# Kernel optimization log

Measured on AMD Instinct MI355X. Metric: run time of the kernel, lower is better.

The kernel has to match this reference:

```python
import jax, jax.numpy as jnp
import numpy as np

IN_C = 512
OUT_C = 1024
N = 8192


def _xavier(key, shape):
    fan_in, fan_out = shape[1], shape[0]
    limit = float(np.sqrt(6.0 / (fan_in + fan_out)))
    return jax.random.uniform(key, shape, jnp.float32, -limit, limit)


def setup_inputs() -> dict:
    key = jax.random.key(0)
    ks = jax.random.split(key, 20)
    inp = {
        'x': jax.random.normal(ks[0], (IN_C, N), jnp.float32),
        'c_prev_dim0': jax.random.normal(ks[1], (OUT_C, N), jnp.float32),
        'h_prev_dim0': jax.random.normal(ks[2], (OUT_C, N), jnp.float32),
        'c_prev_dim1': jax.random.normal(ks[3], (OUT_C, N), jnp.float32),
        'h_prev_dim1': jax.random.normal(ks[4], (OUT_C, N), jnp.float32),
    }
    names_x = ['w_ii', 'w_if', 'w_ig', 'w_io']
    names_h = ['w_hi', 'w_hf', 'w_hg', 'w_ho']
    names_b = ['b_i', 'b_f', 'b_g', 'b_o']
    k = 5
    for n in names_x:
        inp[n] = _xavier(ks[k], (OUT_C, IN_C)); k += 1
    for n in names_h:
        inp[n] = _xavier(ks[k], (OUT_C, OUT_C)); k += 1
    for n in names_b:
        inp[n] = _xavier(ks[k], (OUT_C, 1)); k += 1
    inp['weighted_sum'] = jax.random.uniform(ks[k], (2,), jnp.float32)
    return inp


def reference(x, c_prev_dim0, h_prev_dim0, c_prev_dim1, h_prev_dim1,
              w_ii, w_if, w_ig, w_io,
              w_hi, w_hf, w_hg, w_ho,
              b_i, b_f, b_g, b_o,
              weighted_sum):
    # Input projections shared by both spatial directions: (out, N)
    xi = w_ii @ x
    xf = w_if @ x
    xg = w_ig @ x
    xo = w_io @ x

    def gates(h_prev, c_prev):
        i = jax.nn.sigmoid(xi + w_hi @ h_prev + b_i)
        f = jax.nn.sigmoid(xf + w_hf @ h_prev + b_f)
        g = jnp.tanh(xg + w_hg @ h_prev + b_g)
        o = jax.nn.sigmoid(xo + w_ho @ h_prev + b_o)
        c = f * c_prev + i * g
        h = o * jnp.tanh(c)
        return c, h

    ct0, ht0 = gates(h_prev_dim0, c_prev_dim0)
    ct1, ht1 = gates(h_prev_dim1, c_prev_dim1)
    ct = ct0 * weighted_sum[0] + ct1 * weighted_sum[1]
    ht = ht0 * weighted_sum[0] + ht1 * weighted_sum[1]
    return ct, ht
```

## Files before the change

### kernel.cpp

```cpp
#include <hip/hip_runtime.h>
#include <cstdint>
#include <cstddef>

#define IN_C  512
#define OUT_C 1024
#define NSAMP 8192

#define BM 64
#define BN 64
#define BK 64

typedef __bf16 bf16x8 __attribute__((ext_vector_type(8)));
typedef float  f32x4  __attribute__((ext_vector_type(4)));

__device__ __forceinline__ unsigned short f2bf(float f) {
    unsigned int u = __float_as_uint(f);
    u += 0x7FFFu + ((u >> 16) & 1u);
    return (unsigned short)(u >> 16);
}

__device__ __forceinline__ float sigmoid_f(float x) {
    return 1.0f / (1.0f + __expf(-x));
}
__device__ __forceinline__ float tanh_f(float x) {
    float e = __expf(2.0f * x);
    return 1.0f - 2.0f / (e + 1.0f);
}

__global__ void tcvt_kernel(const float* __restrict__ in, unsigned short* __restrict__ out,
                            int R, int C) {
    __shared__ float t[32][33];
    const int tx = threadIdx.x;
    const int ty = threadIdx.y;
    const int c0 = blockIdx.x * 32;
    const int r0 = blockIdx.y * 32;
#pragma unroll
    for (int i = 0; i < 4; ++i)
        t[ty + i * 8][tx] = in[(size_t)(r0 + ty + i * 8) * C + (c0 + tx)];
    __syncthreads();
#pragma unroll
    for (int i = 0; i < 4; ++i)
        out[(size_t)(c0 + ty + i * 8) * R + (r0 + tx)] = f2bf(t[tx][ty + i * 8]);
}

__global__ void cvt_kernel(const float* __restrict__ in, unsigned short* __restrict__ out, int n4) {
    int idx = blockIdx.x * blockDim.x + threadIdx.x;
    if (idx < n4) {
        float4 v = reinterpret_cast<const float4*>(in)[idx];
        ushort4 o;
        o.x = f2bf(v.x); o.y = f2bf(v.y); o.z = f2bf(v.z); o.w = f2bf(v.w);
        reinterpret_cast<ushort4*>(out)[idx] = o;
    }
}

__global__ __launch_bounds__(256, 2) void mdlstm_main(
    const unsigned short* __restrict__ xT,
    const unsigned short* __restrict__ h0T,
    const unsigned short* __restrict__ h1T,
    const unsigned short* __restrict__ wx,
    const unsigned short* __restrict__ wh,
    const float* __restrict__ b_i, const float* __restrict__ b_f,
    const float* __restrict__ b_g, const float* __restrict__ b_o,
    const float* __restrict__ cp0, const float* __restrict__ cp1,
    const float* __restrict__ wsum,
    float* __restrict__ out)
{
    __shared__ __align__(16) unsigned char smem[6 * 8192];

    const int tid  = threadIdx.x;
    const int lane = tid & 63;
    const int wid  = tid >> 6;
    const int wm   = wid >> 1;
    const int wn   = wid & 1;
    const int g4   = lane >> 4;
    const int l16  = lane & 15;

    const int brow = blockIdx.y * BM;
    const int bcol = blockIdx.x * BN;

    f32x4 acc[2][4][2][2];
#pragma unroll
    for (int d = 0; d < 2; ++d)
#pragma unroll
        for (int q = 0; q < 4; ++q)
#pragma unroll
            for (int a = 0; a < 2; ++a)
#pragma unroll
                for (int b = 0; b < 2; ++b)
                    acc[d][q][a][b] = (f32x4){0.f, 0.f, 0.f, 0.f};

    auto stage_tile = [&](const unsigned short* gbase, int pitch_bytes, int k0bytes, int lds_base) {
#pragma unroll
        for (int j = 0; j < 2; ++j) {
            const int slot = wid * 2 + j;
            const int u    = slot * 1024 + lane * 16;
            const int row  = u >> 7;
            const int kb   = u & 127;
            const char* src = (const char*)gbase + (size_t)row * pitch_bytes + k0bytes
                              + (kb ^ ((row & 7) << 4));
            __builtin_amdgcn_global_load_lds((const unsigned int*)src,
                                             (unsigned int*)(smem + lds_base + slot * 1024),
                                             16, 0, 0);
        }
    };

    auto frag_at = [&](int lds_base, int row, int kbyte) -> bf16x8 {
        const int off = lds_base + row * 128 + (kbyte ^ ((row & 7) << 4));
        return *reinterpret_cast<const bf16x8*>(smem + off);
    };

    for (int st = 0; st < IN_C / BK; ++st) {
        const int k0b = st * BK * 2;
#pragma unroll
        for (int q = 0; q < 4; ++q)
            stage_tile(wx + (size_t)q * OUT_C * IN_C + (size_t)brow * IN_C, IN_C * 2, k0b, q * 8192);
        stage_tile(xT + (size_t)bcol * IN_C, IN_C * 2, k0b, 4 * 8192);
        __syncthreads();
#pragma unroll
        for (int kk = 0; kk < 2; ++kk) {
            const int kbyte = kk * 64 + g4 * 16;
            bf16x8 afr[4][2], bfr[2];
#pragma unroll
            for (int q = 0; q < 4; ++q)
#pragma unroll
                for (int fm = 0; fm < 2; ++fm)
                    afr[q][fm] = frag_at(q * 8192, wm * 32 + fm * 16 + l16, kbyte);
#pragma unroll
            for (int fn = 0; fn < 2; ++fn)
                bfr[fn] = frag_at(4 * 8192, wn * 32 + fn * 16 + l16, kbyte);
#pragma unroll
            for (int q = 0; q < 4; ++q)
#pragma unroll
                for (int fm = 0; fm < 2; ++fm)
#pragma unroll
                    for (int fn = 0; fn < 2; ++fn)
                        acc[0][q][fm][fn] = __builtin_amdgcn_mfma_f32_16x16x32_bf16(
                            afr[q][fm], bfr[fn], acc[0][q][fm][fn], 0, 0, 0);
        }
        __syncthreads();
    }

#pragma unroll
    for (int q = 0; q < 4; ++q)
#pragma unroll
        for (int a = 0; a < 2; ++a)
#pragma unroll
            for (int b = 0; b < 2; ++b)
                acc[1][q][a][b] = acc[0][q][a][b];

    for (int st = 0; st < OUT_C / BK; ++st) {
        const int k0b = st * BK * 2;
#pragma unroll
        for (int q = 0; q < 4; ++q)
            stage_tile(wh + (size_t)q * OUT_C * OUT_C + (size_t)brow * OUT_C, OUT_C * 2, k0b, q * 8192);
        stage_tile(h0T + (size_t)bcol * OUT_C, OUT_C * 2, k0b, 4 * 8192);
        stage_tile(h1T + (size_t)bcol * OUT_C, OUT_C * 2, k0b, 5 * 8192);
        __syncthreads();
#pragma unroll
        for (int kk = 0; kk < 2; ++kk) {
            const int kbyte = kk * 64 + g4 * 16;
            bf16x8 afr[4][2], b0f[2], b1f[2];
#pragma unroll
            for (int q = 0; q < 4; ++q)
#pragma unroll
                for (int fm = 0; fm < 2; ++fm)
                    afr[q][fm] = frag_at(q * 8192, wm * 32 + fm * 16 + l16, kbyte);
#pragma unroll
            for (int fn = 0; fn < 2; ++fn) {
                b0f[fn] = frag_at(4 * 8192, wn * 32 + fn * 16 + l16, kbyte);
                b1f[fn] = frag_at(5 * 8192, wn * 32 + fn * 16 + l16, kbyte);
            }
#pragma unroll
            for (int q = 0; q < 4; ++q)
#pragma unroll
                for (int fm = 0; fm < 2; ++fm)
#pragma unroll
                    for (int fn = 0; fn < 2; ++fn) {
                        acc[0][q][fm][fn] = __builtin_amdgcn_mfma_f32_16x16x32_bf16(
                            afr[q][fm], b0f[fn], acc[0][q][fm][fn], 0, 0, 0);
                        acc[1][q][fm][fn] = __builtin_amdgcn_mfma_f32_16x16x32_bf16(
                            afr[q][fm], b1f[fn], acc[1][q][fm][fn], 0, 0, 0);
                    }
        }
        __syncthreads();
    }

    const float w0 = wsum[0], w1 = wsum[1];
#pragma unroll
    for (int fm = 0; fm < 2; ++fm)
#pragma unroll
        for (int fn = 0; fn < 2; ++fn)
#pragma unroll
            for (int r = 0; r < 4; ++r) {
                const int m = brow + wm * 32 + fm * 16 + g4 * 4 + r;
                const int n = bcol + wn * 32 + fn * 16 + l16;
                const size_t idx = (size_t)m * NSAMP + n;
                const float bi = b_i[m], bff = b_f[m], bg = b_g[m], bo = b_o[m];

                float c0v, h0v, c1v, h1v;
                {
                    float i_ = sigmoid_f(acc[0][0][fm][fn][r] + bi);
                    float f_ = sigmoid_f(acc[0][1][fm][fn][r] + bff);
                    float g_ = tanh_f   (acc[0][2][fm][fn][r] + bg);
                    float o_ = sigmoid_f(acc[0][3][fm][fn][r] + bo);
                    float c_ = f_ * cp0[idx] + i_ * g_;
                    c0v = c_;
                    h0v = o_ * tanh_f(c_);
                }
                {
                    float i_ = sigmoid_f(acc[1][0][fm][fn][r] + bi);
                    float f_ = sigmoid_f(acc[1][1][fm][fn][r] + bff);
                    float g_ = tanh_f   (acc[1][2][fm][fn][r] + bg);
                    float o_ = sigmoid_f(acc[1][3][fm][fn][r] + bo);
                    float c_ = f_ * cp1[idx] + i_ * g_;
                    c1v = c_;
                    h1v = o_ * tanh_f(c_);
                }
                out[idx] = w0 * c0v + w1 * c1v;
                out[(size_t)OUT_C * NSAMP + idx] = w0 * h0v + w1 * h1v;
            }
}

extern "C" void kernel_launch(void* const* d_in, const int* in_sizes, int n_in,
                              void* d_out, int out_size, void* d_ws, size_t ws_size,
                              hipStream_t stream) {
    (void)in_sizes; (void)n_in; (void)out_size; (void)ws_size;

    const float* x    = (const float*)d_in[0];
    const float* cp0  = (const float*)d_in[1];
    const float* hp0  = (const float*)d_in[2];
    const float* cp1  = (const float*)d_in[3];
    const float* hp1  = (const float*)d_in[4];
    const float* wxp[4] = {(const float*)d_in[5], (const float*)d_in[6],
                           (const float*)d_in[7], (const float*)d_in[8]};
    const float* whp[4] = {(const float*)d_in[9], (const float*)d_in[10],
                           (const float*)d_in[11], (const float*)d_in[12]};
    const float* b_i  = (const float*)d_in[13];
    const float* b_f  = (const float*)d_in[14];
    const float* b_g  = (const float*)d_in[15];
    const float* b_o  = (const float*)d_in[16];
    const float* wsum = (const float*)d_in[17];
    float* out = (float*)d_out;

    char* ws = (char*)d_ws;
    unsigned short* xT  = (unsigned short*)(ws);
    unsigned short* h0T = (unsigned short*)(ws + (size_t)8  * 1024 * 1024);
    unsigned short* h1T = (unsigned short*)(ws + (size_t)24 * 1024 * 1024);
    unsigned short* wxc = (unsigned short*)(ws + (size_t)40 * 1024 * 1024);
    unsigned short* whc = (unsigned short*)(ws + (size_t)44 * 1024 * 1024);

    dim3 tb(32, 8);
    tcvt_kernel<<<dim3(NSAMP / 32, IN_C  / 32), tb, 0, stream>>>(x,   xT,  IN_C,  NSAMP);
    tcvt_kernel<<<dim3(NSAMP / 32, OUT_C / 32), tb, 0, stream>>>(hp0, h0T, OUT_C, NSAMP);
    tcvt_kernel<<<dim3(NSAMP / 32, OUT_C / 32), tb, 0, stream>>>(hp1, h1T, OUT_C, NSAMP);

    for (int q = 0; q < 4; ++q)
        cvt_kernel<<<(OUT_C * IN_C / 4) / 256, 256, 0, stream>>>(
            wxp[q], wxc + (size_t)q * OUT_C * IN_C, OUT_C * IN_C / 4);
    for (int q = 0; q < 4; ++q)
        cvt_kernel<<<(OUT_C * OUT_C / 4) / 256, 256, 0, stream>>>(
            whp[q], whc + (size_t)q * OUT_C * OUT_C, OUT_C * OUT_C / 4);

    mdlstm_main<<<dim3(NSAMP / BN, OUT_C / BM), 256, 0, stream>>>(
        xT, h0T, h1T, wxc, whc, b_i, b_f, b_g, b_o, cp0, cp1, wsum, out);
}
```

Baseline: 250.2 us.

## Pack gate weights into unified K=1536 matrix and pipeline 256x128 tile GEMM

Concatenates the x and h weights of all four gates into one row-interleaved bf16 matrix with K=1536, packed by a single kernel. The main kernel becomes one larger-tile GEMM (256 gate rows by 128 samples for both directions) running 512 threads, with double-buffered LDS staging via global_load_lds, explicit vmcnt waits, barriers and setprio around the MFMAs. The two directions are reduced through LDS in the epilogue. The aim is more data reuse per tile, fewer launches, and overlap of memory with compute. The cost is 128KB of LDS per block, which limits occupancy, and hand-tuned synchronization that is fragile.

```diff
diff --git a/kernel.cpp b/kernel.cpp
--- a/kernel.cpp
+++ b/kernel.cpp
@@ -5,23 +5,19 @@
 #define IN_C  512
 #define OUT_C 1024
 #define NSAMP 8192
-
-#define BM 64
-#define BN 64
-#define BK 64
+#define KTOT  1536
 
 typedef __bf16 bf16x8 __attribute__((ext_vector_type(8)));
 typedef float  f32x4  __attribute__((ext_vector_type(4)));
+
+#define SBAR() __builtin_amdgcn_s_barrier()
 
 __device__ __forceinline__ unsigned short f2bf(float f) {
     unsigned int u = __float_as_uint(f);
     u += 0x7FFFu + ((u >> 16) & 1u);
     return (unsigned short)(u >> 16);
 }
-
-__device__ __forceinline__ float sigmoid_f(float x) {
-    return 1.0f / (1.0f + __expf(-x));
-}
+__device__ __forceinline__ float sigmoid_f(float x) { return 1.0f / (1.0f + __expf(-x)); }
 __device__ __forceinline__ float tanh_f(float x) {
     float e = __expf(2.0f * x);
     return 1.0f - 2.0f / (e + 1.0f);
@@ -30,10 +26,8 @@
 __global__ void tcvt_kernel(const float* __restrict__ in, unsigned short* __restrict__ out,
                             int R, int C) {
     __shared__ float t[32][33];
-    const int tx = threadIdx.x;
-    const int ty = threadIdx.y;
-    const int c0 = blockIdx.x * 32;
-    const int r0 = blockIdx.y * 32;
+    const int tx = threadIdx.x, ty = threadIdx.y;
+    const int c0 = blockIdx.x * 32, r0 = blockIdx.y * 32;
 #pragma unroll
     for (int i = 0; i < 4; ++i)
         t[ty + i * 8][tx] = in[(size_t)(r0 + ty + i * 8) * C + (c0 + tx)];
@@ -43,182 +37,210 @@
         out[(size_t)(c0 + ty + i * 8) * R + (r0 + tx)] = f2bf(t[tx][ty + i * 8]);
 }
 
-__global__ void cvt_kernel(const float* __restrict__ in, unsigned short* __restrict__ out, int n4) {
-    int idx = blockIdx.x * blockDim.x + threadIdx.x;
-    if (idx < n4) {
-        float4 v = reinterpret_cast<const float4*>(in)[idx];
-        ushort4 o;
-        o.x = f2bf(v.x); o.y = f2bf(v.y); o.z = f2bf(v.z); o.w = f2bf(v.w);
-        reinterpret_cast<ushort4*>(out)[idx] = o;
-    }
-}
-
-__global__ __launch_bounds__(256, 2) void mdlstm_main(
+__global__ void packA_kernel(const float* __restrict__ x0, const float* __restrict__ x1,
+                             const float* __restrict__ x2, const float* __restrict__ x3,
+                             const float* __restrict__ h0, const float* __restrict__ h1,
+                             const float* __restrict__ h2, const float* __restrict__ h3,
+                             unsigned short* __restrict__ Ap) {
+    const int idx = blockIdx.x * 256 + threadIdx.x;
+    const int m = idx / 192, k8 = idx % 192;
+    const int g = m & 3, r = m >> 2;
+    const float* src;
+    if (k8 < 64) {
+        const float* a = (g & 2) ? ((g & 1) ? x3 : x2) : ((g & 1) ? x1 : x0);
+        src = a + (size_t)r * IN_C + k8 * 8;
+    } else {
+        const float* a = (g & 2) ? ((g & 1) ? h3 : h2) : ((g & 1) ? h1 : h0);
+        src = a + (size_t)r * OUT_C + (k8 - 64) * 8;
+    }
+    float4 v0 = reinterpret_cast<const float4*>(src)[0];
+    float4 v1 = reinterpret_cast<const float4*>(src)[1];
+    ushort4 o0, o1;
+    o0.x = f2bf(v0.x); o0.y = f2bf(v0.y); o0.z = f2bf(v0.z); o0.w = f2bf(v0.w);
+    o1.x = f2bf(v1.x); o1.y = f2bf(v1.y); o1.z = f2bf(v1.z); o1.w = f2bf(v1.w);
+    ushort4* dst = reinterpret_cast<ushort4*>(Ap + (size_t)m * KTOT + k8 * 8);
+    dst[0] = o0; dst[1] = o1;
+}
+
+__global__ __launch_bounds__(512, 2) void mdlstm_main(
+    const unsigned short* __restrict__ Ap,
     const unsigned short* __restrict__ xT,
     const unsigned short* __restrict__ h0T,
     const unsigned short* __restrict__ h1T,
-    const unsigned short* __restrict__ wx,
-    const unsigned short* __restrict__ wh,
     const float* __restrict__ b_i, const float* __restrict__ b_f,
     const float* __restrict__ b_g, const float* __restrict__ b_o,
     const float* __restrict__ cp0, const float* __restrict__ cp1,
     const float* __restrict__ wsum,
     float* __restrict__ out)
 {
-    __shared__ __align__(16) unsigned char smem[6 * 8192];
+    __shared__ __align__(16) unsigned char smem[131072];
 
     const int tid  = threadIdx.x;
     const int lane = tid & 63;
     const int wid  = tid >> 6;
-    const int wm   = wid >> 1;
-    const int wn   = wid & 1;
+    const int wm   = wid >> 2;
+    const int wn   = wid & 3;
     const int g4   = lane >> 4;
     const int l16  = lane & 15;
 
-    const int brow = blockIdx.y * BM;
-    const int bcol = blockIdx.x * BN;
-
-    f32x4 acc[2][4][2][2];
-#pragma unroll
-    for (int d = 0; d < 2; ++d)
-#pragma unroll
-        for (int q = 0; q < 4; ++q)
-#pragma unroll
-            for (int a = 0; a < 2; ++a)
-#pragma unroll
-                for (int b = 0; b < 2; ++b)
-                    acc[d][q][a][b] = (f32x4){0.f, 0.f, 0.f, 0.f};
-
-    auto stage_tile = [&](const unsigned short* gbase, int pitch_bytes, int k0bytes, int lds_base) {
-#pragma unroll
-        for (int j = 0; j < 2; ++j) {
-            const int slot = wid * 2 + j;
-            const int u    = slot * 1024 + lane * 16;
-            const int row  = u >> 7;
-            const int kb   = u & 127;
-            const char* src = (const char*)gbase + (size_t)row * pitch_bytes + k0bytes
-                              + (kb ^ ((row & 7) << 4));
+    const int by    = blockIdx.y;
+    const int bcol  = blockIdx.x * 128;
+    const int browM = by * 256;
+
+    f32x4 acc[8][4];
+#pragma unroll
+    for (int mf = 0; mf < 8; ++mf)
+#pragma unroll
+        for (int nf = 0; nf < 4; ++nf)
+            acc[mf][nf] = (f32x4){0.f, 0.f, 0.f, 0.f};
+
+    auto stage_A = [&](int P, int hA, int j1) {
+#pragma unroll
+        for (int c = 0; c < 2; ++c) {
+            const int u    = c * 8192 + tid * 16;
+            const int rloc = (u >> 6) & 127;
+            const int kb   = (u & 63) ^ (((u >> 7) & 3) << 4);
+            const char* src = (const char*)Ap
+                + ((size_t)(browM + hA * 128 + rloc) * KTOT + j1 * 64 + c * 32) * 2 + kb;
             __builtin_amdgcn_global_load_lds((const unsigned int*)src,
-                                             (unsigned int*)(smem + lds_base + slot * 1024),
-                                             16, 0, 0);
-        }
-    };
-
-    auto frag_at = [&](int lds_base, int row, int kbyte) -> bf16x8 {
-        const int off = lds_base + row * 128 + (kbyte ^ ((row & 7) << 4));
-        return *reinterpret_cast<const bf16x8*>(smem + off);
-    };
-
-    for (int st = 0; st < IN_C / BK; ++st) {
-        const int k0b = st * BK * 2;
-#pragma unroll
-        for (int q = 0; q < 4; ++q)
-            stage_tile(wx + (size_t)q * OUT_C * IN_C + (size_t)brow * IN_C, IN_C * 2, k0b, q * 8192);
-        stage_tile(xT + (size_t)bcol * IN_C, IN_C * 2, k0b, 4 * 8192);
-        __syncthreads();
-#pragma unroll
-        for (int kk = 0; kk < 2; ++kk) {
-            const int kbyte = kk * 64 + g4 * 16;
-            bf16x8 afr[4][2], bfr[2];
-#pragma unroll
-            for (int q = 0; q < 4; ++q)
-#pragma unroll
-                for (int fm = 0; fm < 2; ++fm)
-                    afr[q][fm] = frag_at(q * 8192, wm * 32 + fm * 16 + l16, kbyte);
-#pragma unroll
-            for (int fn = 0; fn < 2; ++fn)
-                bfr[fn] = frag_at(4 * 8192, wn * 32 + fn * 16 + l16, kbyte);
-#pragma unroll
-            for (int q = 0; q < 4; ++q)
-#pragma unroll
-                for (int fm = 0; fm < 2; ++fm)
-#pragma unroll
-                    for (int fn = 0; fn < 2; ++fn)
-                        acc[0][q][fm][fn] = __builtin_amdgcn_mfma_f32_16x16x32_bf16(
-                            afr[q][fm], bfr[fn], acc[0][q][fm][fn], 0, 0, 0);
-        }
-        __syncthreads();
-    }
-
-#pragma unroll
-    for (int q = 0; q < 4; ++q)
-#pragma unroll
-        for (int a = 0; a < 2; ++a)
-#pragma unroll
-            for (int b = 0; b < 2; ++b)
-                acc[1][q][a][b] = acc[0][q][a][b];
-
-    for (int st = 0; st < OUT_C / BK; ++st) {
-        const int k0b = st * BK * 2;
-#pragma unroll
-        for (int q = 0; q < 4; ++q)
-            stage_tile(wh + (size_t)q * OUT_C * OUT_C + (size_t)brow * OUT_C, OUT_C * 2, k0b, q * 8192);
-        stage_tile(h0T + (size_t)bcol * OUT_C, OUT_C * 2, k0b, 4 * 8192);
-        stage_tile(h1T + (size_t)bcol * OUT_C, OUT_C * 2, k0b, 5 * 8192);
-        __syncthreads();
-#pragma unroll
-        for (int kk = 0; kk < 2; ++kk) {
-            const int kbyte = kk * 64 + g4 * 16;
-            bf16x8 afr[4][2], b0f[2], b1f[2];
-#pragma unroll
-            for (int q = 0; q < 4; ++q)
-#pragma unroll
-                for (int fm = 0; fm < 2; ++fm)
-                    afr[q][fm] = frag_at(q * 8192, wm * 32 + fm * 16 + l16, kbyte);
-#pragma unroll
-            for (int fn = 0; fn < 2; ++fn) {
-                b0f[fn] = frag_at(4 * 8192, wn * 32 + fn * 16 + l16, kbyte);
-                b1f[fn] = frag_at(5 * 8192, wn * 32 + fn * 16 + l16, kbyte);
+                (unsigned int*)(smem + P * 65536 + hA * 16384 + u), 16, 0, 0);
+        }
+    };
+    auto stage_B = [&](int P, int d, int j2) {
+#pragma unroll
+        for (int c = 0; c < 2; ++c) {
+            const int u    = c * 8192 + tid * 16;
+            const int rloc = (u >> 6) & 127;
+            const int kb   = (u & 63) ^ (((u >> 7) & 3) << 4);
+            const char* src;
+            if (j2 < 8) {
+                src = (const char*)xT + ((size_t)(bcol + rloc) * IN_C + j2 * 64 + c * 32) * 2 + kb;
+            } else {
+                const unsigned short* hsrc = d ? h1T : h0T;
+                src = (const char*)hsrc + ((size_t)(bcol + rloc) * OUT_C + (j2 - 8) * 64 + c * 32) * 2 + kb;
             }
-#pragma unroll
-            for (int q = 0; q < 4; ++q)
-#pragma unroll
-                for (int fm = 0; fm < 2; ++fm)
-#pragma unroll
-                    for (int fn = 0; fn < 2; ++fn) {
-                        acc[0][q][fm][fn] = __builtin_amdgcn_mfma_f32_16x16x32_bf16(
-                            afr[q][fm], b0f[fn], acc[0][q][fm][fn], 0, 0, 0);
-                        acc[1][q][fm][fn] = __builtin_amdgcn_mfma_f32_16x16x32_bf16(
-                            afr[q][fm], b1f[fn], acc[1][q][fm][fn], 0, 0, 0);
-                    }
-        }
-        __syncthreads();
+            __builtin_amdgcn_global_load_lds((const unsigned int*)src,
+                (unsigned int*)(smem + P * 65536 + 32768 + d * 16384 + u), 16, 0, 0);
+        }
+    };
+
+    auto swzb = [](int u) { return u ^ (((u >> 7) & 3) << 4); };
+    auto fragA = [&](int P, int mf, int kk) -> bf16x8 {
+        const int u = kk * 8192 + (mf * 16 + l16) * 64 + g4 * 16;
+        return *reinterpret_cast<const bf16x8*>(smem + P * 65536 + wm * 16384 + swzb(u));
+    };
+    auto fragB = [&](int P, int nf, int kk) -> bf16x8 {
+        const int u = kk * 8192 + ((wn & 1) * 64 + nf * 16 + l16) * 64 + g4 * 16;
+        return *reinterpret_cast<const bf16x8*>(smem + P * 65536 + 32768 + (wn >> 1) * 16384 + swzb(u));
+    };
+
+    auto ktile = [&](int j, int P, int PN, bool stA, bool stB, bool tail) {
+        bf16x8 bF[4][2], aF[2][2];
+        auto mfma_pair = [&](int M) {
+            __builtin_amdgcn_s_setprio(1);
+#pragma unroll
+            for (int kk = 0; kk < 2; ++kk)
+#pragma unroll
+                for (int mi = 0; mi < 2; ++mi)
+#pragma unroll
+                    for (int nf = 0; nf < 4; ++nf)
+                        acc[M + mi][nf] = __builtin_amdgcn_mfma_f32_16x16x32_bf16(
+                            aF[mi][kk], bF[nf][kk], acc[M + mi][nf], 0, 0, 0);
+            __builtin_amdgcn_s_setprio(0);
+        };
+#pragma unroll
+        for (int nf = 0; nf < 4; ++nf) { bF[nf][0] = fragB(P, nf, 0); bF[nf][1] = fragB(P, nf, 1); }
+#pragma unroll
+        for (int kk = 0; kk < 2; ++kk) { aF[0][kk] = fragA(P, 0, kk); aF[1][kk] = fragA(P, 1, kk); }
+        if (stA) stage_A(PN, 0, j + 1);
+        SBAR();
+        mfma_pair(0);
+        SBAR();
+#pragma unroll
+        for (int kk = 0; kk < 2; ++kk) { aF[0][kk] = fragA(P, 2, kk); aF[1][kk] = fragA(P, 3, kk); }
+        if (stA) stage_A(PN, 1, j + 1);
+        SBAR();
+        mfma_pair(2);
+        SBAR();
+#pragma unroll
+        for (int kk = 0; kk < 2; ++kk) { aF[0][kk] = fragA(P, 4, kk); aF[1][kk] = fragA(P, 5, kk); }
+        if (stB) stage_B(P, 0, j + 2);
+        SBAR();
+        mfma_pair(4);
+        SBAR();
+#pragma unroll
+        for (int kk = 0; kk < 2; ++kk) { aF[0][kk] = fragA(P, 6, kk); aF[1][kk] = fragA(P, 7, kk); }
+        if (stB) stage_B(P, 1, j + 2);
+        SBAR();
+        mfma_pair(6);
+        if (!tail) asm volatile("s_waitcnt vmcnt(4)");
+        else       asm volatile("s_waitcnt vmcnt(0)");
+        SBAR();
+    };
+
+    stage_A(0, 0, 0); stage_A(0, 1, 0);
+    stage_B(0, 0, 0); stage_B(0, 1, 0);
+    stage_B(1, 0, 1); stage_B(1, 1, 1);
+    asm volatile("s_waitcnt vmcnt(4)");
+    SBAR();
+
+#pragma unroll 1
+    for (int jj = 0; jj < 12; ++jj) {
+        const bool s = (jj < 11);
+        ktile(2 * jj,     0, 1, true, s, !s);
+        ktile(2 * jj + 1, 1, 0, s,    s, !s);
     }
 
     const float w0 = wsum[0], w1 = wsum[1];
-#pragma unroll
-    for (int fm = 0; fm < 2; ++fm)
-#pragma unroll
-        for (int fn = 0; fn < 2; ++fn)
-#pragma unroll
-            for (int r = 0; r < 4; ++r) {
-                const int m = brow + wm * 32 + fm * 16 + g4 * 4 + r;
-                const int n = bcol + wn * 32 + fn * 16 + l16;
-                const size_t idx = (size_t)m * NSAMP + n;
-                const float bi = b_i[m], bff = b_f[m], bg = b_g[m], bo = b_o[m];
-
-                float c0v, h0v, c1v, h1v;
-                {
-                    float i_ = sigmoid_f(acc[0][0][fm][fn][r] + bi);
-                    float f_ = sigmoid_f(acc[0][1][fm][fn][r] + bff);
-                    float g_ = tanh_f   (acc[0][2][fm][fn][r] + bg);
-                    float o_ = sigmoid_f(acc[0][3][fm][fn][r] + bo);
-                    float c_ = f_ * cp0[idx] + i_ * g_;
-                    c0v = c_;
-                    h0v = o_ * tanh_f(c_);
-                }
-                {
-                    float i_ = sigmoid_f(acc[1][0][fm][fn][r] + bi);
-                    float f_ = sigmoid_f(acc[1][1][fm][fn][r] + bff);
-                    float g_ = tanh_f   (acc[1][2][fm][fn][r] + bg);
-                    float o_ = sigmoid_f(acc[1][3][fm][fn][r] + bo);
-                    float c_ = f_ * cp1[idx] + i_ * g_;
-                    c1v = c_;
-                    h1v = o_ * tanh_f(c_);
-                }
-                out[idx] = w0 * c0v + w1 * c1v;
-                out[(size_t)OUT_C * NSAMP + idx] = w0 * h0v + w1 * h1v;
+    const int   d  = wn >> 1;
+    const float* cp = d ? cp1 : cp0;
+    const float wd  = d ? w1 : w0;
+
+    float rc[8][4], rh[8][4];
+#pragma unroll
+    for (int mf = 0; mf < 8; ++mf) {
+        const int orow = by * 64 + wm * 32 + mf * 4 + g4;
+        const float bi = b_i[orow], bff = b_f[orow], bg = b_g[orow], bo = b_o[orow];
+#pragma unroll
+        for (int nf = 0; nf < 4; ++nf) {
+            const int scol = bcol + (wn & 1) * 64 + nf * 16 + l16;
+            float i_ = sigmoid_f(acc[mf][nf][0] + bi);
+            float f_ = sigmoid_f(acc[mf][nf][1] + bff);
+            float g_ = tanh_f  (acc[mf][nf][2] + bg);
+            float o_ = sigmoid_f(acc[mf][nf][3] + bo);
+            float cc = f_ * cp[(size_t)orow * NSAMP + scol] + i_ * g_;
+            float hh = o_ * tanh_f(cc);
+            rc[mf][nf] = wd * cc;
+            rh[mf][nf] = wd * hh;
+        }
+    }
+
+    float* ex = (float*)smem;
+    const int rbase = (wm * 2 + (wn & 1)) * 4096;
+    if (d == 1) {
+#pragma unroll
+        for (int mf = 0; mf < 8; ++mf)
+#pragma unroll
+            for (int nf = 0; nf < 4; ++nf) {
+                const int slot = rbase + (mf * 4 + nf) * 64 + lane;
+                ex[slot]        = rc[mf][nf];
+                ex[slot + 2048] = rh[mf][nf];
             }
+    }
+    SBAR();
+    if (d == 0) {
+#pragma unroll
+        for (int mf = 0; mf < 8; ++mf) {
+            const int orow = by * 64 + wm * 32 + mf * 4 + g4;
+#pragma unroll
+            for (int nf = 0; nf < 4; ++nf) {
+                const int scol = bcol + (wn & 1) * 64 + nf * 16 + l16;
+                const int slot = rbase + (mf * 4 + nf) * 64 + lane;
+                out[(size_t)orow * NSAMP + scol] = rc[mf][nf] + ex[slot];
+                out[(size_t)OUT_C * NSAMP + (size_t)orow * NSAMP + scol] = rh[mf][nf] + ex[slot + 2048];
+            }
+        }
+    }
 }
 
 extern "C" void kernel_launch(void* const* d_in, const int* in_sizes, int n_in,
@@ -231,10 +253,6 @@
     const float* hp0  = (const float*)d_in[2];
     const float* cp1  = (const float*)d_in[3];
     const float* hp1  = (const float*)d_in[4];
-    const float* wxp[4] = {(const float*)d_in[5], (const float*)d_in[6],
-                           (const float*)d_in[7], (const float*)d_in[8]};
-    const float* whp[4] = {(const float*)d_in[9], (const float*)d_in[10],
-                           (const float*)d_in[11], (const float*)d_in[12]};
     const float* b_i  = (const float*)d_in[13];
     const float* b_f  = (const float*)d_in[14];
     const float* b_g  = (const float*)d_in[15];
@@ -246,21 +264,18 @@
     unsigned short* xT  = (unsigned short*)(ws);
     unsigned short* h0T = (unsigned short*)(ws + (size_t)8  * 1024 * 1024);
     unsigned short* h1T = (unsigned short*)(ws + (size_t)24 * 1024 * 1024);
-    unsigned short* wxc = (unsigned short*)(ws + (size_t)40 * 1024 * 1024);
-    unsigned short* whc = (unsigned short*)(ws + (size_t)44 * 1024 * 1024);
+    unsigned short* Ap  = (unsigned short*)(ws + (size_t)40 * 1024 * 1024);
 
     dim3 tb(32, 8);
     tcvt_kernel<<<dim3(NSAMP / 32, IN_C  / 32), tb, 0, stream>>>(x,   xT,  IN_C,  NSAMP);
     tcvt_kernel<<<dim3(NSAMP / 32, OUT_C / 32), tb, 0, stream>>>(hp0, h0T, OUT_C, NSAMP);
     tcvt_kernel<<<dim3(NSAMP / 32, OUT_C / 32), tb, 0, stream>>>(hp1, h1T, OUT_C, NSAMP);
 
-    for (int q = 0; q < 4; ++q)
-        cvt_kernel<<<(OUT_C * IN_C / 4) / 256, 256, 0, stream>>>(
-            wxp[q], wxc + (size_t)q * OUT_C * IN_C, OUT_C * IN_C / 4);
-    for (int q = 0; q < 4; ++q)
-        cvt_kernel<<<(OUT_C * OUT_C / 4) / 256, 256, 0, stream>>>(
-            whp[q], whc + (size_t)q * OUT_C * OUT_C, OUT_C * OUT_C / 4);
-
-    mdlstm_main<<<dim3(NSAMP / BN, OUT_C / BM), 256, 0, stream>>>(
-        xT, h0T, h1T, wxc, whc, b_i, b_f, b_g, b_o, cp0, cp1, wsum, out);
-}
+    packA_kernel<<<(4096 * 192) / 256, 256, 0, stream>>>(
+        (const float*)d_in[5], (const float*)d_in[6], (const float*)d_in[7], (const float*)d_in[8],
+        (const float*)d_in[9], (const float*)d_in[10], (const float*)d_in[11], (const float*)d_in[12],
+        Ap);
+
+    mdlstm_main<<<dim3(NSAMP / 128, OUT_C / 64), 512, 0, stream>>>(
+        Ap, xT, h0T, h1T, b_i, b_f, b_g, b_o, cp0, cp1, wsum, out);
+}
```

Measured after the change: 256.2 us. +2.4%, slower.
